# Optimization experiments

Hardware: AMD Instinct MI355X
Metric: run time of the kernel (lower is better)

## Reference

```python
import jax, jax.numpy as jnp
import numpy as np

B, Ca, Cv, NH = 4, 128, 512, 8
Ta, F, Tv = 64, 64, 256
EPS = 1e-5


def group_norm(x, gamma, beta):
    # num_groups=1 GroupNorm: normalize over all non-batch axes, per-channel affine.
    axes = tuple(range(1, x.ndim))
    mu = jnp.mean(x, axis=axes, keepdims=True)
    var = jnp.mean((x - mu) ** 2, axis=axes, keepdims=True)
    xn = (x - mu) * jax.lax.rsqrt(var + EPS)
    shape = (1, -1) + (1,) * (x.ndim - 2)
    return xn * gamma.reshape(shape) + beta.reshape(shape)


def setup_inputs() -> dict:
    key = jax.random.key(0)
    ks = jax.random.split(key, 10)
    s = 0.1
    inp = {
        'audio': jax.random.normal(ks[0], (B, Ca, Ta, F), jnp.float32),
        'video': jax.random.normal(ks[1], (B, Cv, Tv), jnp.float32),
        # grouped 1x1 convs have weight shape (Cout,1,1[,1]) -> flatten to (Cout,)
        'p1_w': jax.random.normal(ks[2], (Cv,), jnp.float32) * s,
        'p1_b': jnp.zeros((Cv,), jnp.float32),
        'p1_g': jnp.ones((Cv,), jnp.float32),
        'p1_be': jnp.zeros((Cv,), jnp.float32),
        'p2_w': jax.random.normal(ks[3], (Cv,), jnp.float32) * s,
        'p2_b': jnp.zeros((Cv,), jnp.float32),
        'p2_g': jnp.ones((Cv,), jnp.float32),
        'p2_be': jnp.zeros((Cv,), jnp.float32),
        'f1_w': jax.random.normal(ks[4], (Cv * NH,), jnp.float32) * s,
        'f1_b': jnp.zeros((Cv * NH,), jnp.float32),
        'f1_g': jnp.ones((Cv * NH,), jnp.float32),
        'f1_be': jnp.zeros((Cv * NH,), jnp.float32),
        'f2_w': jax.random.normal(ks[5], (Cv,), jnp.float32) * s,
        'f2_b': jnp.zeros((Cv,), jnp.float32),
        'f2_g': jnp.ones((Cv,), jnp.float32),
        'f2_be': jnp.zeros((Cv,), jnp.float32),
    }
    return inp


def reference(audio, video, p1_w, p1_b, p1_g, p1_be, p2_w, p2_b, p2_g, p2_be,
              f1_w, f1_b, f1_g, f1_be, f2_w, f2_b, f2_g, f2_be):
    Bx, Cax, Tax, Fx = audio.shape
    _, Cvx, Tvx = video.shape
    rep = Cvx // Cax
    Hx = f1_w.shape[0] // Cvx

    # grouped 1x1 Conv2d (groups=Ca): out channel c reads input channel c // rep
    a_exp = jnp.repeat(audio, rep, axis=1)                      # (B, Cv, Ta, F)
    a_val = group_norm(a_exp * p1_w[None, :, None, None] + p1_b[None, :, None, None], p1_g, p1_be)
    a_gate = jax.nn.relu(group_norm(a_exp * p2_w[None, :, None, None] + p2_b[None, :, None, None], p2_g, p2_be))

    # nearest interpolation Ta -> Tv (F unchanged): src = floor(dst * Ta / Tv)
    idx = (jnp.arange(Tvx) * Tax) // Tvx
    a_val = a_val[:, :, idx, :]                                  # (B, Cv, Tv, F)
    a_gate = a_gate[:, :, idx, :]

    # grouped 1x1 Conv1d f1 (groups=Cv, out=Cv*H): out channel g*H+h reads channel g
    v_rep = jnp.repeat(video, Hx, axis=1)                        # (B, Cv*H, Tv)
    vh = group_norm(v_rep * f1_w[None, :, None] + f1_b[None, :, None], f1_g, f1_be)
    vh = vh.reshape(Bx, Cvx, Hx, Tvx)
    vm = jnp.mean(vh, axis=2)                                    # (B, Cv, Tv)
    v_attn = jax.nn.softmax(vm, axis=-1)

    # grouped 1x1 Conv1d f2 (groups=Cv): per-channel scale
    v_key = group_norm(video * f2_w[None, :, None] + f2_b[None, :, None], f2_g, f2_be)

    fusion = jnp.sum(a_val * v_attn[..., None] + a_gate * v_key[..., None], axis=-1)  # (B, Cv, Tv)
    return fusion + video
```

## Files before the change

### kernel.cpp

```cpp
#include <hip/hip_runtime.h>

#define NB 4
#define CA 128
#define CV 512
#define NHH 8
#define TA 64
#define FF 64
#define TV 256
#define REPC 4
#define EPSV 1e-5f


__device__ __forceinline__ float waveReduceSum(float x) {
  #pragma unroll
  for (int off = 32; off; off >>= 1) x += __shfl_xor(x, off);
  return x;
}
__device__ __forceinline__ float waveReduceMax(float x) {
  #pragma unroll
  for (int off = 32; off; off >>= 1) x = fmaxf(x, __shfl_xor(x, off));
  return x;
}
__device__ __forceinline__ float group4ReduceSum(float x) {
  x += __shfl_xor(x, 1);
  x += __shfl_xor(x, 2);
  return x;
}

__global__ __launch_bounds__(256) void stats_kernel(
    const float* __restrict__ audio, const float* __restrict__ video,
    const float* __restrict__ p1_w, const float* __restrict__ p1_b,
    const float* __restrict__ p2_w, const float* __restrict__ p2_b,
    const float* __restrict__ f1_w, const float* __restrict__ f1_b,
    const float* __restrict__ f2_w, const float* __restrict__ f2_b,
    float* __restrict__ ws)
{
  const int bid = blockIdx.x;
  const int b = bid >> 7, ca = bid & (CA - 1);
  const int c0 = ca * 4;
  const int tid = threadIdx.x;
  const int wv = tid >> 6, ln = tid & 63;
  const int c = c0 + wv;
  __shared__ float red1[4], red2[4], fold[4][4];

  const float4* ap4 = (const float4*)(audio + (size_t)(b * CA + ca) * (TA * FF));
  float4 a0 = ap4[tid];
  float4 a1 = ap4[tid + 256];
  float4 a2 = ap4[tid + 512];
  float4 a3 = ap4[tid + 768];
  const float4* vp4 = (const float4*)(video + (size_t)(b * CV + c) * TV);
  float4 v = vp4[ln];

  float s = a0.x + a0.y + a0.z + a0.w + a1.x + a1.y + a1.z + a1.w
          + a2.x + a2.y + a2.z + a2.w + a3.x + a3.y + a3.z + a3.w;
  float q = a0.x * a0.x + a0.y * a0.y + a0.z * a0.z + a0.w * a0.w
          + a1.x * a1.x + a1.y * a1.y + a1.z * a1.z + a1.w * a1.w
          + a2.x * a2.x + a2.y * a2.y + a2.z * a2.z + a2.w * a2.w
          + a3.x * a3.x + a3.y * a3.y + a3.z * a3.z + a3.w * a3.w;
  s = waveReduceSum(s); q = waveReduceSum(q);
  if (ln == 0) { red1[wv] = s; red2[wv] = q; }

  float vs = v.x + v.y + v.z + v.w;
  float vq = v.x * v.x + v.y * v.y + v.z * v.z + v.w * v.w;
  vs = waveReduceSum(vs); vq = waveReduceSum(vq);
  if (ln == 0) {
    float Wf = 0, Wfq = 0, Wfb = 0, Cf = 0, Cfq = 0;
    #pragma unroll
    for (int h = 0; h < NHH; ++h) {
      int j = c * NHH + h;
      float fw = f1_w[j], fb = f1_b[j];
      Wf += fw; Wfq += fw * fw; Wfb += fw * fb; Cf += fb; Cfq += fb * fb;
    }
    const float NT = (float)TV;
    float w2 = f2_w[c], b2 = f2_b[c];
    fold[wv][0] = Wf * vs + NT * Cf;
    fold[wv][1] = Wfq * vq + 2.f * Wfb * vs + NT * Cfq;
    fold[wv][2] = w2 * vs + NT * b2;
    fold[wv][3] = w2 * w2 * vq + 2.f * w2 * b2 * vs + NT * b2 * b2;
  }
  __syncthreads();
  if (tid == 0) {
    float S = red1[0] + red1[1] + red1[2] + red1[3];
    float Q = red2[0] + red2[1] + red2[2] + red2[3];
    float W1 = 0, W1q = 0, W1pb = 0, C1 = 0, C1q = 0;
    float W2 = 0, W2q = 0, W2pb = 0, C2 = 0, C2q = 0;
    #pragma unroll
    for (int r = 0; r < REPC; ++r) {
      int c2 = c0 + r;
      float w = p1_w[c2], bb = p1_b[c2];
      W1 += w; W1q += w * w; W1pb += w * bb; C1 += bb; C1q += bb * bb;
      float w2 = p2_w[c2], b2 = p2_b[c2];
      W2 += w2; W2q += w2 * w2; W2pb += w2 * b2; C2 += b2; C2q += b2 * b2;
    }
    const float NE = (float)(TA * FF);
    const int base = b * 128 + ca;
    ws[0 * 512 + base] = W1 * S + NE * C1;
    ws[1 * 512 + base] = W1q * Q + 2.f * W1pb * S + NE * C1q;
    ws[2 * 512 + base] = W2 * S + NE * C2;
    ws[3 * 512 + base] = W2q * Q + 2.f * W2pb * S + NE * C2q;
  }
  if (tid >= 4 && tid < 8) {
    int k = tid - 4;
    float p = fold[0][k] + fold[1][k] + fold[2][k] + fold[3][k];
    ws[(4 + k) * 512 + b * 128 + ca] = p;
  }
}

__global__ __launch_bounds__(256) void out_kernel(
    const float* __restrict__ audio, const float* __restrict__ video,
    const float* __restrict__ p1_w, const float* __restrict__ p1_b,
    const float* __restrict__ p1_g, const float* __restrict__ p1_be,
    const float* __restrict__ p2_w, const float* __restrict__ p2_b,
    const float* __restrict__ p2_g, const float* __restrict__ p2_be,
    const float* __restrict__ f1_w, const float* __restrict__ f1_g,
    const float* __restrict__ f2_w, const float* __restrict__ f2_b,
    const float* __restrict__ f2_g, const float* __restrict__ f2_be,
    const float* __restrict__ ws, float* __restrict__ out)
{
  const int bid = blockIdx.x;
  const int b = bid >> 7;
  const int ca = bid & (CA - 1);
  const int c0 = ca * 4;
  const int tid = threadIdx.x;
  const int wv = tid >> 6, ln = tid & 63;
  const int c = c0 + wv;
  const int row = wv * 16 + (ln >> 2);
  const int lq = ln & 3;

  __shared__ float acc8[8];
  __shared__ float ssa[TA];
  __shared__ float sg[4][TA];

  const float4* ap4 = (const float4*)(audio + (size_t)(b * CA + ca) * (TA * FF));
  const int abase = row * 16 + lq;
  float4 av0 = ap4[abase];
  float4 av1 = ap4[abase + 4];
  float4 av2 = ap4[abase + 8];
  float4 av3 = ap4[abase + 12];
  const float4* vp4 = (const float4*)(video + (size_t)(b * CV + c) * TV);
  float4 v = vp4[ln];
  float4 p2w4  = ((const float4*)p2_w)[ca];
  float4 p2b4  = ((const float4*)p2_b)[ca];
  float4 p2g4  = ((const float4*)p2_g)[ca];
  float4 p2be4 = ((const float4*)p2_be)[ca];
  float p1wv = p1_w[c], p1bv = p1_b[c], p1gv = p1_g[c], p1bev = p1_be[c];
  float4 f1wa = ((const float4*)f1_w)[c * 2], f1wb = ((const float4*)f1_w)[c * 2 + 1];
  float4 f1ga = ((const float4*)f1_g)[c * 2], f1gb = ((const float4*)f1_g)[c * 2 + 1];
  float f2wv = f2_w[c], f2bv = f2_b[c], f2gv = f2_g[c], f2bev = f2_be[c];

  #pragma unroll
  for (int r = 0; r < 2; ++r) {
    int qq = wv * 2 + r;
    const float* p = ws + qq * 512 + b * 128;
    float s = p[ln] + p[64 + ln];
    s = waveReduceSum(s);
    if (ln == 0) acc8[qq] = s;
  }
  __syncthreads();

  const float invNa = 1.f / (float)(CV * TA * FF);
  const float invN3 = 1.f / (float)(CV * NHH * TV);
  const float invN4 = 1.f / (float)(CV * TV);
  float mu1 = acc8[0] * invNa;
  float rs1 = rsqrtf(fmaxf(acc8[1] * invNa - mu1 * mu1, 0.f) + EPSV);
  float mu2 = acc8[2] * invNa;
  float rs2 = rsqrtf(fmaxf(acc8[3] * invNa - mu2 * mu2, 0.f) + EPSV);
  float mu3 = acc8[4] * invN3;
  float rs3 = rsqrtf(fmaxf(acc8[5] * invN3 - mu3 * mu3, 0.f) + EPSV);
  float mu4 = acc8[6] * invN4;
  float rs4 = rsqrtf(fmaxf(acc8[7] * invN4 - mu4 * mu4, 0.f) + EPSV);

  float A2a[4], B2a[4];
  A2a[0] = p2w4.x * rs2 * p2g4.x;  B2a[0] = (p2b4.x - mu2) * rs2 * p2g4.x + p2be4.x;
  A2a[1] = p2w4.y * rs2 * p2g4.y;  B2a[1] = (p2b4.y - mu2) * rs2 * p2g4.y + p2be4.y;
  A2a[2] = p2w4.z * rs2 * p2g4.z;  B2a[2] = (p2b4.z - mu2) * rs2 * p2g4.z + p2be4.z;
  A2a[3] = p2w4.w * rs2 * p2g4.w;  B2a[3] = (p2b4.w - mu2) * rs2 * p2g4.w + p2be4.w;

  float sa = av0.x + av0.y + av0.z + av0.w + av1.x + av1.y + av1.z + av1.w
           + av2.x + av2.y + av2.z + av2.w + av3.x + av3.y + av3.z + av3.w;
  float g[4];
  #pragma unroll
  for (int cc = 0; cc < 4; ++cc) {
    float A = A2a[cc], Bv = B2a[cc];
    g[cc] = fmaxf(av0.x * A + Bv, 0.f) + fmaxf(av0.y * A + Bv, 0.f)
          + fmaxf(av0.z * A + Bv, 0.f) + fmaxf(av0.w * A + Bv, 0.f)
          + fmaxf(av1.x * A + Bv, 0.f) + fmaxf(av1.y * A + Bv, 0.f)
          + fmaxf(av1.z * A + Bv, 0.f) + fmaxf(av1.w * A + Bv, 0.f)
          + fmaxf(av2.x * A + Bv, 0.f) + fmaxf(av2.y * A + Bv, 0.f)
          + fmaxf(av2.z * A + Bv, 0.f) + fmaxf(av2.w * A + Bv, 0.f)
          + fmaxf(av3.x * A + Bv, 0.f) + fmaxf(av3.y * A + Bv, 0.f)
          + fmaxf(av3.z * A + Bv, 0.f) + fmaxf(av3.w * A + Bv, 0.f);
  }
  sa = group4ReduceSum(sa);
  g[0] = group4ReduceSum(g[0]);
  g[1] = group4ReduceSum(g[1]);
  g[2] = group4ReduceSum(g[2]);
  g[3] = group4ReduceSum(g[3]);
  if (lq == 0) {
    ssa[row] = sa;
    sg[0][row] = g[0]; sg[1][row] = g[1]; sg[2][row] = g[2]; sg[3][row] = g[3];
  }

  const float A1 = p1wv * rs1 * p1gv;
  const float B1 = (p1bv - mu1) * rs1 * p1gv + p1bev;
  float sw = f1wa.x * f1ga.x + f1wa.y * f1ga.y + f1wa.z * f1ga.z + f1wa.w * f1ga.w
           + f1wb.x * f1gb.x + f1wb.y * f1gb.y + f1wb.z * f1gb.z + f1wb.w * f1gb.w;
  const float alpha = rs3 * sw * (1.f / NHH);
  const float A4 = f2wv * rs4 * f2gv;
  const float B4 = (f2bv - mu4) * rs4 * f2gv + f2bev;

  __syncthreads();

  float l0 = alpha * v.x, l1 = alpha * v.y, l2 = alpha * v.z, l3 = alpha * v.w;
  float m = waveReduceMax(fmaxf(fmaxf(l0, l1), fmaxf(l2, l3)));
  float e0 = __expf(l0 - m), e1 = __expf(l1 - m), e2 = __expf(l2 - m), e3 = __expf(l3 - m);
  float z = waveReduceSum(e0 + e1 + e2 + e3);
  float iz = 1.f / z;
  float sval = A1 * ssa[ln] + (float)FF * B1;
  float sgate = sg[wv][ln];
  float4 o;
  o.x = e0 * iz * sval + (v.x * A4 + B4) * sgate + v.x;
  o.y = e1 * iz * sval + (v.y * A4 + B4) * sgate + v.y;
  o.z = e2 * iz * sval + (v.z * A4 + B4) * sgate + v.z;
  o.w = e3 * iz * sval + (v.w * A4 + B4) * sgate + v.w;
  ((float4*)(out + (size_t)(b * CV + c) * TV))[ln] = o;
}

extern "C" void kernel_launch(void* const* d_in, const int* in_sizes, int n_in,
                              void* d_out, int out_size, void* d_ws, size_t ws_size,
                              hipStream_t stream) {
  const float* audio = (const float*)d_in[0];
  const float* video = (const float*)d_in[1];
  const float* p1_w  = (const float*)d_in[2];
  const float* p1_b  = (const float*)d_in[3];
  const float* p1_g  = (const float*)d_in[4];
  const float* p1_be = (const float*)d_in[5];
  const float* p2_w  = (const float*)d_in[6];
  const float* p2_b  = (const float*)d_in[7];
  const float* p2_g  = (const float*)d_in[8];
  const float* p2_be = (const float*)d_in[9];
  const float* f1_w  = (const float*)d_in[10];
  const float* f1_b  = (const float*)d_in[11];
  const float* f1_g  = (const float*)d_in[12];
  const float* f2_w  = (const float*)d_in[14];
  const float* f2_b  = (const float*)d_in[15];
  const float* f2_g  = (const float*)d_in[16];
  const float* f2_be = (const float*)d_in[17];
  (void)in_sizes; (void)n_in; (void)out_size; (void)ws_size;

  float* ws  = (float*)d_ws;
  float* out = (float*)d_out;

  stats_kernel<<<NB * CA, 256, 0, stream>>>(
      audio, video, p1_w, p1_b, p2_w, p2_b, f1_w, f1_b, f2_w, f2_b, ws);

  out_kernel<<<NB * CA, 256, 0, stream>>>(
      audio, video,
      p1_w, p1_b, p1_g, p1_be,
      p2_w, p2_b, p2_g, p2_be,
      f1_w, f1_g, f2_w, f2_b, f2_g, f2_be,
      ws, out);
}
```

Baseline: 14.33 us.

## Fuse stats and output kernels with a software grid barrier

Merges the statistics kernel and the output kernel into one launch. A global atomic barrier separates the stats phase from the normalization/output phase, and audio and video tiles stay in registers across both phases so they are not reloaded. This removes one kernel launch and the second read of the inputs. In exchange it relies on all 512 blocks being co-resident, which is not guaranteed, and on spin-waiting, with a barrier counter reset scheme that could race across back-to-back launches.

```diff
diff --git a/kernel.cpp b/kernel.cpp
--- a/kernel.cpp
+++ b/kernel.cpp
@@ -9,7 +9,11 @@
 #define TV 256
 #define REPC 4
 #define EPSV 1e-5f
-
+#define GRID (NB * CA)
+
+
+__device__ unsigned g_arrive = 0u;
+__device__ unsigned g_obs    = 0u;
 
 __device__ __forceinline__ float waveReduceSum(float x) {
   #pragma unroll
@@ -27,13 +31,17 @@
   return x;
 }
 
-__global__ __launch_bounds__(256) void stats_kernel(
+__global__ __launch_bounds__(256, 2) void fused_kernel(
     const float* __restrict__ audio, const float* __restrict__ video,
     const float* __restrict__ p1_w, const float* __restrict__ p1_b,
+    const float* __restrict__ p1_g, const float* __restrict__ p1_be,
     const float* __restrict__ p2_w, const float* __restrict__ p2_b,
+    const float* __restrict__ p2_g, const float* __restrict__ p2_be,
     const float* __restrict__ f1_w, const float* __restrict__ f1_b,
+    const float* __restrict__ f1_g,
     const float* __restrict__ f2_w, const float* __restrict__ f2_b,
-    float* __restrict__ ws)
+    const float* __restrict__ f2_g, const float* __restrict__ f2_be,
+    float* __restrict__ ws, float* __restrict__ out)
 {
   const int bid = blockIdx.x;
   const int b = bid >> 7, ca = bid & (CA - 1);
@@ -41,22 +49,37 @@
   const int tid = threadIdx.x;
   const int wv = tid >> 6, ln = tid & 63;
   const int c = c0 + wv;
-  __shared__ float red1[4], red2[4], fold[4][4];
+  const int row = wv * 16 + (ln >> 2);
+  const int lq = ln & 3;
+
+  __shared__ float red1[4], red2[4], fold[4][4], acc8[8];
+  __shared__ float ssa[TA];
+  __shared__ float sg[4][TA];
 
   const float4* ap4 = (const float4*)(audio + (size_t)(b * CA + ca) * (TA * FF));
-  float4 a0 = ap4[tid];
-  float4 a1 = ap4[tid + 256];
-  float4 a2 = ap4[tid + 512];
-  float4 a3 = ap4[tid + 768];
+  const int abase = row * 16 + lq;
+  float4 av0 = ap4[abase];
+  float4 av1 = ap4[abase + 4];
+  float4 av2 = ap4[abase + 8];
+  float4 av3 = ap4[abase + 12];
   const float4* vp4 = (const float4*)(video + (size_t)(b * CV + c) * TV);
   float4 v = vp4[ln];
-
-  float s = a0.x + a0.y + a0.z + a0.w + a1.x + a1.y + a1.z + a1.w
-          + a2.x + a2.y + a2.z + a2.w + a3.x + a3.y + a3.z + a3.w;
-  float q = a0.x * a0.x + a0.y * a0.y + a0.z * a0.z + a0.w * a0.w
-          + a1.x * a1.x + a1.y * a1.y + a1.z * a1.z + a1.w * a1.w
-          + a2.x * a2.x + a2.y * a2.y + a2.z * a2.z + a2.w * a2.w
-          + a3.x * a3.x + a3.y * a3.y + a3.z * a3.z + a3.w * a3.w;
+  float4 p2w4  = ((const float4*)p2_w)[ca];
+  float4 p2b4  = ((const float4*)p2_b)[ca];
+  float4 p2g4  = ((const float4*)p2_g)[ca];
+  float4 p2be4 = ((const float4*)p2_be)[ca];
+  float p1wv = p1_w[c], p1bv = p1_b[c], p1gv = p1_g[c], p1bev = p1_be[c];
+  float4 f1wa = ((const float4*)f1_w)[c * 2], f1wb = ((const float4*)f1_w)[c * 2 + 1];
+  float4 f1ba = ((const float4*)f1_b)[c * 2], f1bb = ((const float4*)f1_b)[c * 2 + 1];
+  float4 f1ga = ((const float4*)f1_g)[c * 2], f1gb = ((const float4*)f1_g)[c * 2 + 1];
+  float f2wv = f2_w[c], f2bv = f2_b[c], f2gv = f2_g[c], f2bev = f2_be[c];
+
+  float s = av0.x + av0.y + av0.z + av0.w + av1.x + av1.y + av1.z + av1.w
+          + av2.x + av2.y + av2.z + av2.w + av3.x + av3.y + av3.z + av3.w;
+  float q = av0.x * av0.x + av0.y * av0.y + av0.z * av0.z + av0.w * av0.w
+          + av1.x * av1.x + av1.y * av1.y + av1.z * av1.z + av1.w * av1.w
+          + av2.x * av2.x + av2.y * av2.y + av2.z * av2.z + av2.w * av2.w
+          + av3.x * av3.x + av3.y * av3.y + av3.z * av3.z + av3.w * av3.w;
   s = waveReduceSum(s); q = waveReduceSum(q);
   if (ln == 0) { red1[wv] = s; red2[wv] = q; }
 
@@ -64,19 +87,19 @@
   float vq = v.x * v.x + v.y * v.y + v.z * v.z + v.w * v.w;
   vs = waveReduceSum(vs); vq = waveReduceSum(vq);
   if (ln == 0) {
-    float Wf = 0, Wfq = 0, Wfb = 0, Cf = 0, Cfq = 0;
-    #pragma unroll
-    for (int h = 0; h < NHH; ++h) {
-      int j = c * NHH + h;
-      float fw = f1_w[j], fb = f1_b[j];
-      Wf += fw; Wfq += fw * fw; Wfb += fw * fb; Cf += fb; Cfq += fb * fb;
-    }
+    float Wf  = f1wa.x + f1wa.y + f1wa.z + f1wa.w + f1wb.x + f1wb.y + f1wb.z + f1wb.w;
+    float Wfq = f1wa.x * f1wa.x + f1wa.y * f1wa.y + f1wa.z * f1wa.z + f1wa.w * f1wa.w
+              + f1wb.x * f1wb.x + f1wb.y * f1wb.y + f1wb.z * f1wb.z + f1wb.w * f1wb.w;
+    float Wfb = f1wa.x * f1ba.x + f1wa.y * f1ba.y + f1wa.z * f1ba.z + f1wa.w * f1ba.w
+              + f1wb.x * f1bb.x + f1wb.y * f1bb.y + f1wb.z * f1bb.z + f1wb.w * f1bb.w;
+    float Cf  = f1ba.x + f1ba.y + f1ba.z + f1ba.w + f1bb.x + f1bb.y + f1bb.z + f1bb.w;
+    float Cfq = f1ba.x * f1ba.x + f1ba.y * f1ba.y + f1ba.z * f1ba.z + f1ba.w * f1ba.w
+              + f1bb.x * f1bb.x + f1bb.y * f1bb.y + f1bb.z * f1bb.z + f1bb.w * f1bb.w;
     const float NT = (float)TV;
-    float w2 = f2_w[c], b2 = f2_b[c];
     fold[wv][0] = Wf * vs + NT * Cf;
     fold[wv][1] = Wfq * vq + 2.f * Wfb * vs + NT * Cfq;
-    fold[wv][2] = w2 * vs + NT * b2;
-    fold[wv][3] = w2 * w2 * vq + 2.f * w2 * b2 * vs + NT * b2 * b2;
+    fold[wv][2] = f2wv * vs + NT * f2bv;
+    fold[wv][3] = f2wv * f2wv * vq + 2.f * f2wv * f2bv * vs + NT * f2bv * f2bv;
   }
   __syncthreads();
   if (tid == 0) {
@@ -104,57 +127,29 @@
     float p = fold[0][k] + fold[1][k] + fold[2][k] + fold[3][k];
     ws[(4 + k) * 512 + b * 128 + ca] = p;
   }
-}
-
-__global__ __launch_bounds__(256) void out_kernel(
-    const float* __restrict__ audio, const float* __restrict__ video,
-    const float* __restrict__ p1_w, const float* __restrict__ p1_b,
-    const float* __restrict__ p1_g, const float* __restrict__ p1_be,
-    const float* __restrict__ p2_w, const float* __restrict__ p2_b,
-    const float* __restrict__ p2_g, const float* __restrict__ p2_be,
-    const float* __restrict__ f1_w, const float* __restrict__ f1_g,
-    const float* __restrict__ f2_w, const float* __restrict__ f2_b,
-    const float* __restrict__ f2_g, const float* __restrict__ f2_be,
-    const float* __restrict__ ws, float* __restrict__ out)
-{
-  const int bid = blockIdx.x;
-  const int b = bid >> 7;
-  const int ca = bid & (CA - 1);
-  const int c0 = ca * 4;
-  const int tid = threadIdx.x;
-  const int wv = tid >> 6, ln = tid & 63;
-  const int c = c0 + wv;
-  const int row = wv * 16 + (ln >> 2);
-  const int lq = ln & 3;
-
-  __shared__ float acc8[8];
-  __shared__ float ssa[TA];
-  __shared__ float sg[4][TA];
-
-  const float4* ap4 = (const float4*)(audio + (size_t)(b * CA + ca) * (TA * FF));
-  const int abase = row * 16 + lq;
-  float4 av0 = ap4[abase];
-  float4 av1 = ap4[abase + 4];
-  float4 av2 = ap4[abase + 8];
-  float4 av3 = ap4[abase + 12];
-  const float4* vp4 = (const float4*)(video + (size_t)(b * CV + c) * TV);
-  float4 v = vp4[ln];
-  float4 p2w4  = ((const float4*)p2_w)[ca];
-  float4 p2b4  = ((const float4*)p2_b)[ca];
-  float4 p2g4  = ((const float4*)p2_g)[ca];
-  float4 p2be4 = ((const float4*)p2_be)[ca];
-  float p1wv = p1_w[c], p1bv = p1_b[c], p1gv = p1_g[c], p1bev = p1_be[c];
-  float4 f1wa = ((const float4*)f1_w)[c * 2], f1wb = ((const float4*)f1_w)[c * 2 + 1];
-  float4 f1ga = ((const float4*)f1_g)[c * 2], f1gb = ((const float4*)f1_g)[c * 2 + 1];
-  float f2wv = f2_w[c], f2bv = f2_b[c], f2gv = f2_g[c], f2bev = f2_be[c];
+  __syncthreads();
+
+  if (tid == 0) {
+    __threadfence();
+    atomicAdd(&g_arrive, 1u);
+    while (__hip_atomic_load(&g_arrive, __ATOMIC_RELAXED, __HIP_MEMORY_SCOPE_AGENT) < GRID)
+      __builtin_amdgcn_s_sleep(1);
+    __threadfence();
+    unsigned o = atomicAdd(&g_obs, 1u);
+    if (o == GRID - 1) {
+      __hip_atomic_store(&g_arrive, 0u, __ATOMIC_RELAXED, __HIP_MEMORY_SCOPE_AGENT);
+      __hip_atomic_store(&g_obs,    0u, __ATOMIC_RELAXED, __HIP_MEMORY_SCOPE_AGENT);
+    }
+  }
+  __syncthreads();
 
   #pragma unroll
   for (int r = 0; r < 2; ++r) {
     int qq = wv * 2 + r;
     const float* p = ws + qq * 512 + b * 128;
-    float s = p[ln] + p[64 + ln];
-    s = waveReduceSum(s);
-    if (ln == 0) acc8[qq] = s;
+    float s2 = p[ln] + p[64 + ln];
+    s2 = waveReduceSum(s2);
+    if (ln == 0) acc8[qq] = s2;
   }
   __syncthreads();
 
@@ -251,13 +246,11 @@
   float* ws  = (float*)d_ws;
   float* out = (float*)d_out;
 
-  stats_kernel<<<NB * CA, 256, 0, stream>>>(
-      audio, video, p1_w, p1_b, p2_w, p2_b, f1_w, f1_b, f2_w, f2_b, ws);
-
-  out_kernel<<<NB * CA, 256, 0, stream>>>(
+  fused_kernel<<<GRID, 256, 0, stream>>>(
       audio, video,
       p1_w, p1_b, p1_g, p1_be,
       p2_w, p2_b, p2_g, p2_be,
-      f1_w, f1_g, f2_w, f2_b, f2_g, f2_be,
+      f1_w, f1_b, f1_g,
+      f2_w, f2_b, f2_g, f2_be,
       ws, out);
 }
```

Result: slower. 44.96 us (+213.7%).
